# Optimization experiments

Hardware: AMD Instinct MI355X
Metric: run time of the kernel (lower is better)

## Reference

```python
import jax, jax.numpy as jnp
import numpy as np

HID, OUT, VOCAB, MSIZE, MDIM = 1024, 512, 1024, 262144, 128


def setup_inputs() -> dict:
    key = jax.random.key(0)
    ks = jax.random.split(key, 16)
    s = lambda i, shape, scale=0.02: jax.random.normal(ks[i], shape, dtype=jnp.float32) * scale
    return {
        "input": s(0, (1, 1, VOCAB), 1.0),
        "hidden0": s(1, (1, 1, HID), 1.0),
        "stack": s(2, (MSIZE, MDIM), 1.0),
        "W_ih": s(3, (HID, VOCAB)),
        "W_hh": s(4, (HID, HID)),
        "b_ih": s(5, (HID,)),
        "b_hh": s(6, (HID,)),
        "W_y": s(7, (OUT, HID)),
        "b_y": s(8, (OUT,)),
        "W_n": s(9, (MDIM, HID)),
        "b_n": s(10, (MDIM,)),
        "W_a": s(11, (2, HID)),
        "b_a": s(12, (2,)),
        "W_sh": s(13, (HID, MDIM)),
        "b_sh": s(14, (HID,)),
    }


def reference(input, hidden0, stack, W_ih, W_hh, b_ih, b_hh, W_y, b_y, W_n, b_n, W_a, b_a, W_sh, b_sh):
    # hidden_bar = W_sh(stack[0]).view(1,1,-1) + hidden0   -> (1,1,H)
    hidden_bar = (stack[0] @ W_sh.T + b_sh)[None, None, :] + hidden0
    # single-step, single-layer tanh RNN cell
    h = jnp.tanh(input @ W_ih.T + b_ih + hidden_bar @ W_hh.T + b_hh)  # (1,1,H)
    output = jax.nn.sigmoid(h @ W_y.T + b_y).reshape(-1, OUT)          # (1,OUT)
    action_weights = jax.nn.softmax(h @ W_a.T + b_a, axis=2).reshape(-1)  # (2,)
    new_elt = jax.nn.sigmoid(h @ W_n.T + b_n).reshape(1, MDIM)         # (1,MDIM)
    push_side = jnp.concatenate([new_elt, stack[:-1]], axis=0)
    pop_side = jnp.concatenate([stack[1:], jnp.zeros((1, MDIM), dtype=stack.dtype)], axis=0)
    new_stack = action_weights[0] * push_side + action_weights[1] * pop_side
    return output, h, new_stack
```

## Files before the change

### kernel.cpp

```cpp
#include <hip/hip_runtime.h>
#include <cmath>

#define HID 1024
#define OUTN 512
#define VOCABN 1024
#define MSIZE 262144
#define MDIM 128

#define WS_TIH 0
#define WS_HB  1024
#define WS_H   2048
#define WS_AW  3072
#define WS_NE  3076

__device__ __forceinline__ float wred(float v) {
#pragma unroll
    for (int m = 32; m; m >>= 1) v += __shfl_xor(v, m, 64);
    return v;
}

__device__ __forceinline__ float dot4(const float4* __restrict__ a,
                                      const float4* __restrict__ b,
                                      int n4, int lane) {
    float acc = 0.f;
    for (int k = lane; k < n4; k += 64) {
        float4 x = a[k], y = b[k];
        acc = fmaf(x.x, y.x, fmaf(x.y, y.y, fmaf(x.z, y.z, fmaf(x.w, y.w, acc))));
    }
    return wred(acc);
}

__device__ __forceinline__ float4 blend4(float aw0, float aw1, float4 push, float4 pop) {
    float4 r;
    r.x = fmaf(aw0, push.x, aw1 * pop.x);
    r.y = fmaf(aw0, push.y, aw1 * pop.y);
    r.z = fmaf(aw0, push.z, aw1 * pop.z);
    r.w = fmaf(aw0, push.w, aw1 * pop.w);
    return r;
}

__global__ void k_pre(const float* __restrict__ input, const float* __restrict__ hidden0,
                      const float* __restrict__ stack, const float* __restrict__ W_ih,
                      const float* __restrict__ b_ih, const float* __restrict__ W_sh,
                      const float* __restrict__ b_sh, float* __restrict__ ws) {
    const int lane = threadIdx.x & 63;
    const int row = blockIdx.x * (blockDim.x >> 6) + (threadIdx.x >> 6);
    if (row >= HID) return;
    float t  = dot4((const float4*)(W_ih + row * VOCABN), (const float4*)input, VOCABN / 4, lane);
    float hb = dot4((const float4*)(W_sh + row * MDIM), (const float4*)stack, MDIM / 4, lane);
    if (lane == 0) {
        ws[WS_TIH + row] = t + b_ih[row];
        ws[WS_HB + row]  = hb + b_sh[row] + hidden0[row];
    }
}

__global__ void k_h(const float* __restrict__ W_hh, const float* __restrict__ b_hh,
                    float* __restrict__ ws, float* __restrict__ d_out) {
    const int lane = threadIdx.x & 63;
    const int row = blockIdx.x * (blockDim.x >> 6) + (threadIdx.x >> 6);
    if (row >= HID) return;
    float a = dot4((const float4*)(W_hh + row * HID), (const float4*)(ws + WS_HB), HID / 4, lane);
    if (lane == 0) {
        float h = tanhf(ws[WS_TIH + row] + a + b_hh[row]);
        ws[WS_H + row] = h;
        d_out[OUTN + row] = h;
    }
}

__global__ void k_heads(const float* __restrict__ W_y, const float* __restrict__ b_y,
                        const float* __restrict__ W_n, const float* __restrict__ b_n,
                        const float* __restrict__ W_a, const float* __restrict__ b_a,
                        float* __restrict__ ws, float* __restrict__ d_out) {
    const int lane = threadIdx.x & 63;
    const int row = blockIdx.x * (blockDim.x >> 6) + (threadIdx.x >> 6);
    const float4* h4 = (const float4*)(ws + WS_H);
    if (row < OUTN) {
        float a = dot4((const float4*)(W_y + row * HID), h4, HID / 4, lane);
        if (lane == 0) d_out[row] = 1.f / (1.f + expf(-(a + b_y[row])));
    } else if (row < OUTN + MDIM) {
        const int m = row - OUTN;
        float a = dot4((const float4*)(W_n + m * HID), h4, HID / 4, lane);
        if (lane == 0) ws[WS_NE + m] = 1.f / (1.f + expf(-(a + b_n[m])));
    } else if (row == OUTN + MDIM) {
        float l0 = dot4((const float4*)(W_a), h4, HID / 4, lane);
        float l1 = dot4((const float4*)(W_a + HID), h4, HID / 4, lane);
        if (lane == 0) {
            l0 += b_a[0];
            l1 += b_a[1];
            const float mx = fmaxf(l0, l1);
            const float e0 = expf(l0 - mx), e1 = expf(l1 - mx);
            const float s = e0 + e1;
            ws[WS_AW]     = e0 / s;
            ws[WS_AW + 1] = e1 / s;
        }
    }
}

__global__ __launch_bounds__(256, 8) void k_stack(
    const float* __restrict__ stack, const float* __restrict__ ws,
    float* __restrict__ out_stack) {
    const float aw0 = ws[WS_AW];
    const float aw1 = ws[WS_AW + 1];
    const float4* s4  = (const float4*)stack;
    const float4* ne4 = (const float4*)(ws + WS_NE);
    float4* o4 = (float4*)out_stack;
    const int total4 = MSIZE * (MDIM / 4);
    const int lane = threadIdx.x & 63;
    const int wid  = blockIdx.x * 4 + (threadIdx.x >> 6);
    const long base = (long)wid * 1024;

    float4 prev;
    if (wid == 0) prev = (lane < 32) ? ne4[lane] : s4[lane - 32];
    else          prev = s4[base - 32 + lane];

#pragma unroll 4
    for (int i = 0; i < 16; ++i) {
        const long A = base + i * 64;
        const long nidx = A + 32 + lane;
        float4 next = make_float4(0.f, 0.f, 0.f, 0.f);
        if (nidx < total4) next = s4[nidx];
        o4[A + lane] = blend4(aw0, aw1, prev, next);
        prev = next;
    }
}

extern "C" void kernel_launch(void* const* d_in, const int* in_sizes, int n_in,
                              void* d_out, int out_size, void* d_ws, size_t ws_size,
                              hipStream_t stream) {
    const float* input   = (const float*)d_in[0];
    const float* hidden0 = (const float*)d_in[1];
    const float* stack   = (const float*)d_in[2];
    const float* W_ih    = (const float*)d_in[3];
    const float* W_hh    = (const float*)d_in[4];
    const float* b_ih    = (const float*)d_in[5];
    const float* b_hh    = (const float*)d_in[6];
    const float* W_y     = (const float*)d_in[7];
    const float* b_y     = (const float*)d_in[8];
    const float* W_n     = (const float*)d_in[9];
    const float* b_n     = (const float*)d_in[10];
    const float* W_a     = (const float*)d_in[11];
    const float* b_a     = (const float*)d_in[12];
    const float* W_sh    = (const float*)d_in[13];
    const float* b_sh    = (const float*)d_in[14];
    float* out = (float*)d_out;
    float* ws  = (float*)d_ws;

    k_pre<<<256, 256, 0, stream>>>(input, hidden0, stack, W_ih, b_ih, W_sh, b_sh, ws);
    k_h<<<256, 256, 0, stream>>>(W_hh, b_hh, ws, out);
    k_heads<<<161, 256, 0, stream>>>(W_y, b_y, W_n, b_n, W_a, b_a, ws, out);
    k_stack<<<2048, 256, 0, stream>>>(stack, ws, out + OUTN + HID);
}
```

Baseline: 68.01 us.

## Fuse hidden_bar and RNN cell kernels with per-block redundant W_sh GEMV

Merges k_pre and k_h into one kernel. Each of the 128 blocks recomputes the full hidden_bar vector (the W_sh times stack[0] product) into shared memory, then computes the input and recurrent dot products for its 8 rows together. This removes one kernel launch and the global round-trip through the workspace. In exchange, every block rereads all 512KB of W_sh, mostly from cache, and does that GEMV with one thread per row, which gives uncoalesced strided loads.

```diff
diff --git a/kernel.cpp b/kernel.cpp
--- a/kernel.cpp
+++ b/kernel.cpp
@@ -7,11 +7,9 @@
 #define MSIZE 262144
 #define MDIM 128
 
-#define WS_TIH 0
-#define WS_HB  1024
-#define WS_H   2048
-#define WS_AW  3072
-#define WS_NE  3076
+#define WS_H   0
+#define WS_AW  1024
+#define WS_NE  1040
 
 __device__ __forceinline__ float wred(float v) {
 #pragma unroll
@@ -39,31 +37,51 @@
     return r;
 }
 
-__global__ void k_pre(const float* __restrict__ input, const float* __restrict__ hidden0,
-                      const float* __restrict__ stack, const float* __restrict__ W_ih,
-                      const float* __restrict__ b_ih, const float* __restrict__ W_sh,
-                      const float* __restrict__ b_sh, float* __restrict__ ws) {
-    const int lane = threadIdx.x & 63;
-    const int row = blockIdx.x * (blockDim.x >> 6) + (threadIdx.x >> 6);
-    if (row >= HID) return;
-    float t  = dot4((const float4*)(W_ih + row * VOCABN), (const float4*)input, VOCABN / 4, lane);
-    float hb = dot4((const float4*)(W_sh + row * MDIM), (const float4*)stack, MDIM / 4, lane);
+__global__ __launch_bounds__(512) void k_fused(
+    const float* __restrict__ stack, const float* __restrict__ hidden0,
+    const float* __restrict__ input, const float* __restrict__ W_sh,
+    const float* __restrict__ b_sh, const float* __restrict__ W_ih,
+    const float* __restrict__ W_hh, const float* __restrict__ b_ih,
+    const float* __restrict__ b_hh, float* __restrict__ ws,
+    float* __restrict__ d_out) {
+    __shared__ __align__(16) float s0[MDIM];
+    __shared__ __align__(16) float hb[HID];
+    const int t = threadIdx.x;
+
+    if (t < 32) ((float4*)s0)[t] = ((const float4*)stack)[t];
+    __syncthreads();
+
+    const float4* s04 = (const float4*)s0;
+    for (int j = t; j < HID; j += 512) {
+        const float4* w = (const float4*)(W_sh + j * MDIM);
+        float acc = 0.f;
+#pragma unroll 8
+        for (int k = 0; k < MDIM / 4; ++k) {
+            const float4 a = w[k], s = s04[k];
+            acc = fmaf(a.x, s.x, fmaf(a.y, s.y, fmaf(a.z, s.z, fmaf(a.w, s.w, acc))));
+        }
+        hb[j] = acc + b_sh[j] + hidden0[j];
+    }
+    __syncthreads();
+
+    const int lane = t & 63;
+    const int R = blockIdx.x * 8 + (t >> 6);
+    const float4* wi  = (const float4*)(W_ih + R * VOCABN);
+    const float4* wh  = (const float4*)(W_hh + R * HID);
+    const float4* in4 = (const float4*)input;
+    const float4* hb4 = (const float4*)hb;
+    float acc = 0.f;
+    for (int k = lane; k < VOCABN / 4; k += 64) {
+        float4 a = wi[k], b = in4[k];
+        acc = fmaf(a.x, b.x, fmaf(a.y, b.y, fmaf(a.z, b.z, fmaf(a.w, b.w, acc))));
+        float4 c = wh[k], d = hb4[k];
+        acc = fmaf(c.x, d.x, fmaf(c.y, d.y, fmaf(c.z, d.z, fmaf(c.w, d.w, acc))));
+    }
+    acc = wred(acc);
     if (lane == 0) {
-        ws[WS_TIH + row] = t + b_ih[row];
-        ws[WS_HB + row]  = hb + b_sh[row] + hidden0[row];
-    }
-}
-
-__global__ void k_h(const float* __restrict__ W_hh, const float* __restrict__ b_hh,
-                    float* __restrict__ ws, float* __restrict__ d_out) {
-    const int lane = threadIdx.x & 63;
-    const int row = blockIdx.x * (blockDim.x >> 6) + (threadIdx.x >> 6);
-    if (row >= HID) return;
-    float a = dot4((const float4*)(W_hh + row * HID), (const float4*)(ws + WS_HB), HID / 4, lane);
-    if (lane == 0) {
-        float h = tanhf(ws[WS_TIH + row] + a + b_hh[row]);
-        ws[WS_H + row] = h;
-        d_out[OUTN + row] = h;
+        const float h = tanhf(acc + b_ih[R] + b_hh[R]);
+        ws[WS_H + R] = h;
+        d_out[OUTN + R] = h;
     }
 }
 
@@ -145,8 +163,8 @@
     float* out = (float*)d_out;
     float* ws  = (float*)d_ws;
 
-    k_pre<<<256, 256, 0, stream>>>(input, hidden0, stack, W_ih, b_ih, W_sh, b_sh, ws);
-    k_h<<<256, 256, 0, stream>>>(W_hh, b_hh, ws, out);
+    k_fused<<<128, 512, 0, stream>>>(stack, hidden0, input, W_sh, b_sh,
+                                     W_ih, W_hh, b_ih, b_hh, ws, out);
     k_heads<<<161, 256, 0, stream>>>(W_y, b_y, W_n, b_n, W_a, b_a, ws, out);
     k_stack<<<2048, 256, 0, stream>>>(stack, ws, out + OUTN + HID);
 }
```

After: 78.92 us. 1.16x slower.
